# Performance work log

Measured on AMD Instinct MI355X. Metric: run time of the kernel, lower is better.

The kernel has to match this reference:

```python
import jax, jax.numpy as jnp
import numpy as np

NEG = -9e15

def setup_inputs() -> dict:
    key = jax.random.key(0)
    k1, k2, k3, k4, k5 = jax.random.split(key, 5)
    N, Fin, Fout = 8192, 256, 128
    h = jax.random.normal(k1, (N, Fin), dtype=jnp.float32)
    adj = jax.random.randint(k2, (N, N), 0, 2, dtype=jnp.int32)
    # Parameters (xavier_uniform with gain=1.414 for a1/a2; kaiming-like for W is fine as random init)
    lim_w = float(np.sqrt(6.0 / (Fin + Fout)))
    W = jax.random.uniform(k3, (Fout, Fin), dtype=jnp.float32, minval=-lim_w, maxval=lim_w)
    lim_a = float(1.414 * np.sqrt(6.0 / (Fout + 1)))
    a1 = jax.random.uniform(k4, (Fout, 1), dtype=jnp.float32, minval=-lim_a, maxval=lim_a)
    a2 = jax.random.uniform(k5, (Fout, 1), dtype=jnp.float32, minval=-lim_a, maxval=lim_a)
    return {"h": h, "adj": adj, "W": W, "a1": a1, "a2": a2}

def reference(h, adj, W, a1, a2):
    Wh = h @ W.T                                   # [N, Fout]
    s1 = (Wh @ a1)                                 # [N, 1]
    s2 = (Wh @ a2)                                 # [N, 1]
    e = jax.nn.leaky_relu(s1 + s2.T, 0.2)          # [N, N]
    att = jnp.where(adj > 0, e, jnp.float32(NEG))
    att = jax.nn.softmax(att, axis=1)
    h_prime = att @ Wh                             # [N, Fout]
    return jax.nn.elu(h_prime)
```

## Files before the change

### kernel.cpp

```cpp
#include <hip/hip_runtime.h>
#include <cstdint>
#include <cstddef>

#define N_NODES 8192
#define FIN 256
#define FOUT 128
#define JS 16
#define JW (N_NODES / JS)
#define KCH (JW / 32)
#define LOG2E 1.4426950408889634f

typedef __attribute__((ext_vector_type(8))) short bf16x8;
typedef __attribute__((ext_vector_type(4))) float f32x4;
typedef __attribute__((ext_vector_type(4))) int i32x4;

__device__ __forceinline__ float bf2f(unsigned short u) {
    union { unsigned int i; float f; } v; v.i = ((unsigned int)u) << 16; return v.f;
}
__device__ __forceinline__ unsigned short f2bf(float f) {
    union { float f; unsigned int i; } v; v.f = f;
    unsigned int r = (v.i + 0x7FFFu + ((v.i >> 16) & 1u)) >> 16;
    return (unsigned short)r;
}
__device__ __forceinline__ unsigned int pack_bf16(float a, float b) {
    return (unsigned)f2bf(a) | ((unsigned)f2bf(b) << 16);
}

__device__ __forceinline__ size_t whb_idx(int j, int f) {
    return ((size_t)((j >> 5) * 8 + (f >> 4)) << 9) + (((j >> 3) & 3) << 7)
         + ((f & 15) << 3) + (j & 7);
}

__global__ __launch_bounds__(256) void wh_kernel(const float* __restrict__ h,
                                                 const float* __restrict__ W,
                                                 unsigned short* __restrict__ whB) {
    __shared__ float hT[64][FIN + 5];
    const int t = threadIdx.x;
    const int i0 = blockIdx.x * 64;
    const int f0 = blockIdx.y * 32;
#pragma unroll
    for (int c = 0; c < 16; ++c) {
        int chunk = c * 256 + t;
        int row = chunk >> 6, col = (chunk & 63) * 4;
        f32x4 v = *(const f32x4*)&h[(size_t)(i0 + row) * FIN + col];
        hT[row][col] = v[0]; hT[row][col + 1] = v[1];
        hT[row][col + 2] = v[2]; hT[row][col + 3] = v[3];
    }
    __syncthreads();
    const int lane = t & 63;
    const int fb8 = __builtin_amdgcn_readfirstlane(f0 + (t >> 6) * 8);
    const float* w0 = W + (size_t)fb8 * FIN;
    float acc[8] = {0.f, 0.f, 0.f, 0.f, 0.f, 0.f, 0.f, 0.f};
    for (int k = 0; k < FIN; k += 4) {
        float h0 = hT[lane][k],     h1 = hT[lane][k + 1];
        float h2 = hT[lane][k + 2], h3 = hT[lane][k + 3];
#pragma unroll
        for (int c = 0; c < 8; ++c) {
            const float* wr = w0 + c * FIN;
            acc[c] += h0 * wr[k] + h1 * wr[k + 1] + h2 * wr[k + 2] + h3 * wr[k + 3];
        }
    }
    const int i = i0 + lane;
#pragma unroll
    for (int c = 0; c < 8; ++c)
        whB[whb_idx(i, fb8 + c)] = f2bf(acc[c]);
}

__global__ __launch_bounds__(256) void s_kernel(const unsigned short* __restrict__ whB,
                                                const float* __restrict__ a1,
                                                const float* __restrict__ a2,
                                                float* __restrict__ s1,
                                                float* __restrict__ s2) {
    __shared__ float p1[4][64], p2[4][64];
    const int t = threadIdx.x;
    const int l = t & 63;
    const int g = t >> 6;
    const int i = blockIdx.x * 64 + l;
    float acc1 = 0.f, acc2 = 0.f;
#pragma unroll
    for (int fb = g * 2; fb < g * 2 + 2; ++fb) {
#pragma unroll
        for (int sl = 0; sl < 16; ++sl) {
            int f = fb * 16 + sl;
            float v = bf2f(whB[whb_idx(i, f)]);
            acc1 += v * a1[f];
            acc2 += v * a2[f];
        }
    }
    p1[g][l] = acc1; p2[g][l] = acc2;
    __syncthreads();
    if (g == 0) {
        s1[i] = (p1[0][l] + p1[1][l] + p1[2][l] + p1[3][l]) * LOG2E;
        s2[i] = (p2[0][l] + p2[1][l] + p2[2][l] + p2[3][l]) * LOG2E;
    }
}

__global__ __launch_bounds__(256) void gat_kernel(const int* __restrict__ adj,
                                                  const unsigned short* __restrict__ whB,
                                                  const float* __restrict__ s1,
                                                  const float* __restrict__ s2,
                                                  float* __restrict__ out,
                                                  float* __restrict__ nums,
                                                  float* __restrict__ dens) {
    const int t = threadIdx.x;
    const int w = t >> 6;
    const int lane = t & 63;
    const int sl = lane & 15;
    const int quad = lane >> 4;
    const int slice = blockIdx.x & (JS - 1);
    const int rg = (blockIdx.x >> 4) * 4 + w;
    const int row0 = rg * 32;
    const int jb = slice * JW;
    float* __restrict__ num = slice ? (nums + (size_t)(slice - 1) * N_NODES * FOUT) : out;
    float* __restrict__ den = dens + (size_t)slice * N_NODES;

    const float s1a = s1[row0 + sl];
    const float s1b = s1[row0 + 16 + sl];
    const int* aR0 = adj + (size_t)(row0 + sl) * N_NODES + jb + quad * 8;
    const int* aR1 = aR0 + (size_t)16 * N_NODES;
    const float* s2p = s2 + jb + quad * 8;

    f32x4 acc[2][8];
#pragma unroll
    for (int m = 0; m < 2; ++m)
#pragma unroll
        for (int fb = 0; fb < 8; ++fb) acc[m][fb] = (f32x4){0.f, 0.f, 0.f, 0.f};

    float d0 = 0.f, d1 = 0.f;

    i32x4 pa0 = *(const i32x4*)(aR0);
    i32x4 pa1 = *(const i32x4*)(aR0 + 4);
    i32x4 pb0 = *(const i32x4*)(aR1);
    i32x4 pb1 = *(const i32x4*)(aR1 + 4);
    f32x4 ps0 = *(const f32x4*)(s2p);
    f32x4 ps1 = *(const f32x4*)(s2p + 4);

#pragma unroll 1
    for (int ch = 0; ch < KCH; ++ch) {
        i32x4 ca0 = pa0, ca1 = pa1, cb0 = pb0, cb1 = pb1;
        f32x4 cs0 = ps0, cs1 = ps1;
        if (ch + 1 < KCH) {
            int o = (ch + 1) * 32;
            pa0 = *(const i32x4*)(aR0 + o);
            pa1 = *(const i32x4*)(aR0 + o + 4);
            pb0 = *(const i32x4*)(aR1 + o);
            pb1 = *(const i32x4*)(aR1 + o + 4);
            ps0 = *(const f32x4*)(s2p + o);
            ps1 = *(const f32x4*)(s2p + o + 4);
        }
        const int kb = jb / 32 + ch;
        const unsigned short* bp = whB + ((size_t)(kb * 8) << 9) + lane * 8;
        bf16x8 Ba[4];
#pragma unroll
        for (int fb = 0; fb < 4; ++fb) Ba[fb] = *(const bf16x8*)(bp + ((size_t)fb << 9));
        float p0[8], p1[8];
#pragma unroll
        for (int e = 0; e < 8; ++e) {
            float sc = (e < 4) ? cs0[e] : cs1[e - 4];
            int m0 = (e < 4) ? ca0[e] : ca1[e - 4];
            int m1 = (e < 4) ? cb0[e] : cb1[e - 4];
            float y0 = s1a + sc;
            float y1 = s1b + sc;
            y0 = fmaxf(y0, 0.2f * y0);
            y1 = fmaxf(y1, 0.2f * y1);
            float e0 = __builtin_amdgcn_exp2f(y0);
            float e1 = __builtin_amdgcn_exp2f(y1);
            p0[e] = (m0 > 0) ? e0 : 0.f;
            p1[e] = (m1 > 0) ? e1 : 0.f;
            d0 += p0[e];
            d1 += p1[e];
        }
        union { bf16x8 v; unsigned int u[4]; } A0, A1;
#pragma unroll
        for (int q = 0; q < 4; ++q) {
            A0.u[q] = pack_bf16(p0[2 * q], p0[2 * q + 1]);
            A1.u[q] = pack_bf16(p1[2 * q], p1[2 * q + 1]);
        }
#pragma unroll
        for (int fb = 0; fb < 4; ++fb) {
            acc[0][fb] = __builtin_amdgcn_mfma_f32_16x16x32_bf16(A0.v, Ba[fb], acc[0][fb], 0, 0, 0);
            acc[1][fb] = __builtin_amdgcn_mfma_f32_16x16x32_bf16(A1.v, Ba[fb], acc[1][fb], 0, 0, 0);
        }
        bf16x8 Bb[4];
#pragma unroll
        for (int fb = 0; fb < 4; ++fb) Bb[fb] = *(const bf16x8*)(bp + ((size_t)(4 + fb) << 9));
#pragma unroll
        for (int fb = 0; fb < 4; ++fb) {
            acc[0][4 + fb] = __builtin_amdgcn_mfma_f32_16x16x32_bf16(A0.v, Bb[fb], acc[0][4 + fb], 0, 0, 0);
            acc[1][4 + fb] = __builtin_amdgcn_mfma_f32_16x16x32_bf16(A1.v, Bb[fb], acc[1][4 + fb], 0, 0, 0);
        }
    }
    d0 += __shfl_xor(d0, 16); d0 += __shfl_xor(d0, 32);
    d1 += __shfl_xor(d1, 16); d1 += __shfl_xor(d1, 32);
    if (lane < 16) {
        den[row0 + lane] = d0;
        den[row0 + 16 + lane] = d1;
    }
#pragma unroll
    for (int m = 0; m < 2; ++m)
#pragma unroll
        for (int fb = 0; fb < 8; ++fb)
#pragma unroll
            for (int r = 0; r < 4; ++r) {
                int row = row0 + m * 16 + quad * 4 + r;
                num[(size_t)row * FOUT + fb * 16 + sl] = acc[m][fb][r];
            }
}

__global__ __launch_bounds__(256) void fin_kernel(float* __restrict__ out,
                                                  const float* __restrict__ nums,
                                                  const float* __restrict__ dens) {
    const int idx = blockIdx.x * 256 + threadIdx.x;
    const int i = idx >> 7;
    const size_t NF = (size_t)N_NODES * FOUT;
    float numv = out[idx];
#pragma unroll
    for (int k = 0; k < JS - 1; ++k) numv += nums[k * NF + idx];
    float denv = 0.f;
#pragma unroll
    for (int k = 0; k < JS; ++k) denv += dens[k * N_NODES + i];
    float v = numv / fmaxf(denv, 1e-30f);
    out[idx] = (v > 0.f) ? v : expm1f(v);
}

extern "C" void kernel_launch(void* const* d_in, const int* in_sizes, int n_in,
                              void* d_out, int out_size, void* d_ws, size_t ws_size,
                              hipStream_t stream) {
    const float* h   = (const float*)d_in[0];
    const int*   adj = (const int*)d_in[1];
    const float* W   = (const float*)d_in[2];
    const float* a1  = (const float*)d_in[3];
    const float* a2  = (const float*)d_in[4];

    char* ws = (char*)d_ws;
    unsigned short* whB = (unsigned short*)ws;
    float* s1   = (float*)(ws + (2u << 20));
    float* s2   = s1 + N_NODES;
    float* dens = s2 + N_NODES;
    float* nums = dens + JS * N_NODES;
    float* out  = (float*)d_out;

    wh_kernel<<<dim3(N_NODES / 64, FOUT / 32), 256, 0, stream>>>(h, W, whB);
    s_kernel<<<dim3(N_NODES / 64), 256, 0, stream>>>(whB, a1, a2, s1, s2);
    gat_kernel<<<dim3((N_NODES / 128) * JS), 256, 0, stream>>>(adj, whB, s1, s2,
                                                               out, nums, dens);
    fin_kernel<<<dim3(N_NODES * FOUT / 256), 256, 0, stream>>>(out, nums, dens);
}
```

Baseline: 443.2 us.

## Pack adjacency into bitmask in a pre-pass and halve column slices

Adds a pack kernel that turns the int32 adjacency matrix into a per-row bitmask using wavefront ballots, so the attention kernel reads one byte per 8 neighbours instead of 32 bytes. It also cuts the column-split count from 16 to 8, which lowers the partial-sum traffic in the final reduction but halves the grid size. The full adjacency still has to be read once by the pack kernel, so the saving comes mainly from making that read coalesced and cheaper than the strided per-lane loads in the main kernel.

```diff
diff --git a/kernel.cpp b/kernel.cpp
--- a/kernel.cpp
+++ b/kernel.cpp
@@ -5,14 +5,13 @@
 #define N_NODES 8192
 #define FIN 256
 #define FOUT 128
-#define JS 16
+#define JS 8
 #define JW (N_NODES / JS)
 #define KCH (JW / 32)
 #define LOG2E 1.4426950408889634f
 
 typedef __attribute__((ext_vector_type(8))) short bf16x8;
 typedef __attribute__((ext_vector_type(4))) float f32x4;
-typedef __attribute__((ext_vector_type(4))) int i32x4;
 
 __device__ __forceinline__ float bf2f(unsigned short u) {
     union { unsigned int i; float f; } v; v.i = ((unsigned int)u) << 16; return v.f;
@@ -29,6 +28,33 @@
 __device__ __forceinline__ size_t whb_idx(int j, int f) {
     return ((size_t)((j >> 5) * 8 + (f >> 4)) << 9) + (((j >> 3) & 3) << 7)
          + ((f & 15) << 3) + (j & 7);
+}
+
+__global__ __launch_bounds__(256) void pack_kernel(const int* __restrict__ adj,
+                                                   unsigned long long* __restrict__ bits) {
+    const int t = threadIdx.x;
+    const int lane = t & 63;
+    const int wv = t >> 6;
+    const int wid = blockIdx.x * 4 + wv;
+#pragma unroll
+    for (int pass = 0; pass < 2; ++pass) {
+        const int row = wid + pass * 4096;
+        const int* ar = adj + (size_t)row * N_NODES;
+        unsigned long long k0 = 0, k1 = 0;
+#pragma unroll
+        for (int seg = 0; seg < 64; ++seg) {
+            unsigned long long m = __ballot(ar[seg * 64 + lane] > 0);
+            if (lane == seg) k0 = m;
+        }
+#pragma unroll
+        for (int seg = 0; seg < 64; ++seg) {
+            unsigned long long m = __ballot(ar[4096 + seg * 64 + lane] > 0);
+            if (lane == seg) k1 = m;
+        }
+        unsigned long long* br = bits + (size_t)row * 128;
+        br[lane] = k0;
+        br[64 + lane] = k1;
+    }
 }
 
 __global__ __launch_bounds__(256) void wh_kernel(const float* __restrict__ h,
@@ -95,7 +121,7 @@
     }
 }
 
-__global__ __launch_bounds__(256) void gat_kernel(const int* __restrict__ adj,
+__global__ __launch_bounds__(256) void gat_kernel(const unsigned char* __restrict__ bits8,
                                                   const unsigned short* __restrict__ whB,
                                                   const float* __restrict__ s1,
                                                   const float* __restrict__ s2,
@@ -108,7 +134,7 @@
     const int sl = lane & 15;
     const int quad = lane >> 4;
     const int slice = blockIdx.x & (JS - 1);
-    const int rg = (blockIdx.x >> 4) * 4 + w;
+    const int rg = (blockIdx.x >> 3) * 4 + w;
     const int row0 = rg * 32;
     const int jb = slice * JW;
     float* __restrict__ num = slice ? (nums + (size_t)(slice - 1) * N_NODES * FOUT) : out;
@@ -116,8 +142,8 @@
 
     const float s1a = s1[row0 + sl];
     const float s1b = s1[row0 + 16 + sl];
-    const int* aR0 = adj + (size_t)(row0 + sl) * N_NODES + jb + quad * 8;
-    const int* aR1 = aR0 + (size_t)16 * N_NODES;
+    const unsigned char* bR0 = bits8 + (size_t)(row0 + sl) * (N_NODES / 8) + (jb >> 3) + quad;
+    const unsigned char* bR1 = bR0 + (size_t)16 * (N_NODES / 8);
     const float* s2p = s2 + jb + quad * 8;
 
     f32x4 acc[2][8];
@@ -128,23 +154,19 @@
 
     float d0 = 0.f, d1 = 0.f;
 
-    i32x4 pa0 = *(const i32x4*)(aR0);
-    i32x4 pa1 = *(const i32x4*)(aR0 + 4);
-    i32x4 pb0 = *(const i32x4*)(aR1);
-    i32x4 pb1 = *(const i32x4*)(aR1 + 4);
+    unsigned int pm0 = bR0[0];
+    unsigned int pm1 = bR1[0];
     f32x4 ps0 = *(const f32x4*)(s2p);
     f32x4 ps1 = *(const f32x4*)(s2p + 4);
 
 #pragma unroll 1
     for (int ch = 0; ch < KCH; ++ch) {
-        i32x4 ca0 = pa0, ca1 = pa1, cb0 = pb0, cb1 = pb1;
+        unsigned int cm0 = pm0, cm1 = pm1;
         f32x4 cs0 = ps0, cs1 = ps1;
         if (ch + 1 < KCH) {
             int o = (ch + 1) * 32;
-            pa0 = *(const i32x4*)(aR0 + o);
-            pa1 = *(const i32x4*)(aR0 + o + 4);
-            pb0 = *(const i32x4*)(aR1 + o);
-            pb1 = *(const i32x4*)(aR1 + o + 4);
+            pm0 = bR0[(ch + 1) * 4];
+            pm1 = bR1[(ch + 1) * 4];
             ps0 = *(const f32x4*)(s2p + o);
             ps1 = *(const f32x4*)(s2p + o + 4);
         }
@@ -157,16 +179,14 @@
 #pragma unroll
         for (int e = 0; e < 8; ++e) {
             float sc = (e < 4) ? cs0[e] : cs1[e - 4];
-            int m0 = (e < 4) ? ca0[e] : ca1[e - 4];
-            int m1 = (e < 4) ? cb0[e] : cb1[e - 4];
             float y0 = s1a + sc;
             float y1 = s1b + sc;
             y0 = fmaxf(y0, 0.2f * y0);
             y1 = fmaxf(y1, 0.2f * y1);
             float e0 = __builtin_amdgcn_exp2f(y0);
             float e1 = __builtin_amdgcn_exp2f(y1);
-            p0[e] = (m0 > 0) ? e0 : 0.f;
-            p1[e] = (m1 > 0) ? e1 : 0.f;
+            p0[e] = ((cm0 >> e) & 1u) ? e0 : 0.f;
+            p1[e] = ((cm1 >> e) & 1u) ? e1 : 0.f;
             d0 += p0[e];
             d1 += p1[e];
         }
@@ -233,16 +253,19 @@
     const float* a2  = (const float*)d_in[4];
 
     char* ws = (char*)d_ws;
-    unsigned short* whB = (unsigned short*)ws;
-    float* s1   = (float*)(ws + (2u << 20));
+    unsigned short*     whB  = (unsigned short*)ws;
+    unsigned long long* bits = (unsigned long long*)(ws + (2u << 20));
+    float* s1   = (float*)(ws + (10u << 20));
     float* s2   = s1 + N_NODES;
     float* dens = s2 + N_NODES;
     float* nums = dens + JS * N_NODES;
     float* out  = (float*)d_out;
 
+    pack_kernel<<<dim3(1024), 256, 0, stream>>>(adj, bits);
     wh_kernel<<<dim3(N_NODES / 64, FOUT / 32), 256, 0, stream>>>(h, W, whB);
     s_kernel<<<dim3(N_NODES / 64), 256, 0, stream>>>(whB, a1, a2, s1, s2);
-    gat_kernel<<<dim3((N_NODES / 128) * JS), 256, 0, stream>>>(adj, whB, s1, s2,
-                                                               out, nums, dens);
+    gat_kernel<<<dim3((N_NODES / 128) * JS), 256, 0, stream>>>((const unsigned char*)bits,
+                                                               whB, s1, s2, out,
+                                                               nums, dens);
     fin_kernel<<<dim3(N_NODES * FOUT / 256), 256, 0, stream>>>(out, nums, dens);
 }
```

After: 445.5 us. No clear change (+0.5%).
